# Optimization experiments

Hardware: AMD Instinct MI355X
Metric: run time of the kernel (lower is better)

## Reference

```python
import jax, jax.numpy as jnp
import numpy as np

B, T, D, H = 4, 2048, 1024, 16
HD = D // H

def setup_inputs() -> dict:
    key = jax.random.key(0)
    ks = jax.random.split(key, 5)
    s = 0.02
    return {
        "x": jax.random.normal(ks[0], (B, T, D), dtype=jnp.float32),
        "w_qkv": jax.random.normal(ks[1], (D, 3 * D), dtype=jnp.float32) * s,
        "b_qkv": jax.random.normal(ks[2], (3 * D,), dtype=jnp.float32) * s,
        "w_proj": jax.random.normal(ks[3], (D, D), dtype=jnp.float32) * s,
        "b_proj": jax.random.normal(ks[4], (D,), dtype=jnp.float32) * s,
    }

def reference(x, w_qkv, b_qkv, w_proj, b_proj):
    b, t, c = x.shape
    h, hd = H, HD
    scale = hd ** -0.5
    qkv = x @ w_qkv + b_qkv                       # [B,T,3D]
    qkv = qkv.reshape(b, t, 3, h, hd)
    q, k, v = qkv[:, :, 0], qkv[:, :, 1], qkv[:, :, 2]   # [B,T,H,HD]
    # scores [B,H,T,T]
    att = jnp.einsum('bqhd,bkhd->bhqk', q, k) * scale
    causal = jnp.tril(jnp.ones((t, t), dtype=bool))
    att = jnp.where(causal[None, None], att, -jnp.inf)
    w = jax.nn.softmax(att, axis=-1)
    out = jnp.einsum('bhqk,bkhd->bqhd', w, v).reshape(b, t, c)
    return out @ w_proj + b_proj
```

## Files before the change

### kernel.cpp

```cpp
#include <hip/hip_runtime.h>
#include <hip/hip_bf16.h>
#include <cstdint>

#define BB 4
#define TT 2048
#define DD 1024
#define HH 16
#define HD 64
#define MM (BB*TT)
#define NQKV (3*DD)
#define QSCALE 0.18033688f
#define NQT 16

typedef __bf16 bf16;
typedef __bf16 bf16x8 __attribute__((ext_vector_type(8)));
typedef float f32x4 __attribute__((ext_vector_type(4)));

#define AS1 __attribute__((address_space(1)))
#define AS3 __attribute__((address_space(3)))

__device__ __forceinline__ void gload_lds16(const void* g, void* l) {
  __builtin_amdgcn_global_load_lds((const AS1 uint32_t*)g, (AS3 uint32_t*)l, 16, 0, 0);
}

__global__ void k_prep(const float* __restrict__ x, bf16* __restrict__ xb,
                       const float* __restrict__ wqkv, bf16* __restrict__ wqkvT,
                       const float* __restrict__ wproj, bf16* __restrict__ wprojT) {
  __shared__ float tile[32][33];
  const int bid = blockIdx.x;
  if (bid < 8192) {
    const int i = bid * 256 + threadIdx.x;
    float4 v = ((const float4*)x)[i];
    ushort4 o;
    o.x = __builtin_bit_cast(unsigned short, (bf16)v.x);
    o.y = __builtin_bit_cast(unsigned short, (bf16)v.y);
    o.z = __builtin_bit_cast(unsigned short, (bf16)v.z);
    o.w = __builtin_bit_cast(unsigned short, (bf16)v.w);
    ((ushort4*)xb)[i] = o;
    return;
  }
  const float* in; bf16* out; int R, C, c0, r0;
  if (bid < 8192 + 3072) {
    const int id = bid - 8192;
    in = wqkv; out = wqkvT; R = DD; C = NQKV;
    c0 = (id % 96) * 32; r0 = (id / 96) * 32;
  } else {
    const int id = bid - 8192 - 3072;
    in = wproj; out = wprojT; R = DD; C = DD;
    c0 = (id % 32) * 32; r0 = (id / 32) * 32;
  }
  const int tx = threadIdx.x & 31, ty = threadIdx.x >> 5;
#pragma unroll
  for (int i = 0; i < 32; i += 8)
    tile[ty + i][tx] = in[(long)(r0 + ty + i) * C + c0 + tx];
  __syncthreads();
#pragma unroll
  for (int i = 0; i < 32; i += 8)
    out[(long)(c0 + ty + i) * R + r0 + tx] = (bf16)tile[tx][ty + i];
}

template <int EPI>
__global__ __launch_bounds__(256) void k_gemm(
    const bf16* __restrict__ A, const bf16* __restrict__ Bt,
    const float* __restrict__ bias, float* __restrict__ fout,
    bf16* __restrict__ q_out, bf16* __restrict__ k_out, bf16* __restrict__ v_out,
    int K) {
  __shared__ bf16 sm[2 * 128 * 64];
  bf16* const As = sm;
  bf16* const Bs = sm + 128 * 64;
  const int tid = threadIdx.x;
  const int m0 = blockIdx.x * 128;
  const int n0 = blockIdx.y * 128;
  const int wv = tid >> 6, lane = tid & 63;
  const int g = lane >> 4, lr = lane & 15;
  const int wm = (wv >> 1) * 64, wn = (wv & 1) * 64;
  const int sr = tid >> 3, sc = tid & 7;
  f32x4 acc[4][4] = {};

  for (int k0 = 0; k0 < K; k0 += 64) {
#pragma unroll
    for (int p = 0; p < 4; ++p) {
      const int row = p * 32 + sr;
      const int chunk = sc ^ (row & 7);
      gload_lds16(A + ((long)(m0 + row) * K + k0 + (chunk << 3)),
                  As + (row << 6) + (sc << 3));
      gload_lds16(Bt + ((long)(n0 + row) * K + k0 + (chunk << 3)),
                  Bs + (row << 6) + (sc << 3));
    }
    __syncthreads();
#pragma unroll
    for (int kf = 0; kf < 2; ++kf) {
      bf16x8 af[4], bfr[4];
#pragma unroll
      for (int mf = 0; mf < 4; ++mf) {
        const int row = wm + mf * 16 + lr;
        af[mf] = *(const bf16x8*)((const char*)As +
                 (((row << 7) + (kf << 6) + (g << 4)) ^ ((row & 7) << 4)));
      }
#pragma unroll
      for (int nf = 0; nf < 4; ++nf) {
        const int row = wn + nf * 16 + lr;
        bfr[nf] = *(const bf16x8*)((const char*)Bs +
                 (((row << 7) + (kf << 6) + (g << 4)) ^ ((row & 7) << 4)));
      }
#pragma unroll
      for (int mf = 0; mf < 4; ++mf)
#pragma unroll
        for (int nf = 0; nf < 4; ++nf)
          acc[mf][nf] = __builtin_amdgcn_mfma_f32_16x16x32_bf16(af[mf], bfr[nf],
                                                                acc[mf][nf], 0, 0, 0);
    }
    __syncthreads();
  }

  if (EPI == 0) {
    const int sel = n0 >> 10;
    const int d0 = n0 & 1023;
    const int b = m0 >> 11;
    const int t0 = m0 & 2047;
    const int h0 = d0 >> 6;
    if (sel < 2) {
      const float qs = (sel == 0) ? QSCALE : 1.0f;
      bf16* Cs = sm;
#pragma unroll
      for (int nf = 0; nf < 4; ++nf) {
        const int col = wn + nf * 16 + lr;
        const float bv = bias[n0 + col];
#pragma unroll
        for (int mf = 0; mf < 4; ++mf)
#pragma unroll
          for (int j = 0; j < 4; ++j) {
            const int row = wm + mf * 16 + g * 4 + j;
            const float v = (acc[mf][nf][j] + bv) * qs;
            const int cp = (col >> 3) ^ (((row >> 2) & 3) << 1);
            Cs[(row << 7) + (cp << 3) + (col & 7)] = (bf16)v;
          }
      }
      __syncthreads();
      bf16* dst = (sel == 0) ? q_out : k_out;
#pragma unroll
      for (int i = 0; i < 8; ++i) {
        const int cid = (i << 8) + tid;
        const int hh = cid >> 10;
        const int r  = (cid >> 3) & 127;
        const int ck = cid & 7;
        const int cp = ((hh << 3) + ck) ^ (((r >> 2) & 3) << 1);
        const bf16x8 vv = *(const bf16x8*)&Cs[(r << 7) + (cp << 3)];
        const long off = ((((long)b * HH + h0 + hh) * TT + t0 + r) << 6) + (ck << 3);
        *(bf16x8*)(dst + off) = vv;
      }
    } else {
      bf16* Cs = sm;
#pragma unroll
      for (int nf = 0; nf < 4; ++nf) {
        const int col = wn + nf * 16 + lr;
        const float bv = bias[n0 + col];
#pragma unroll
        for (int mf = 0; mf < 4; ++mf) {
          const int row0 = wm + mf * 16 + g * 4;
          ushort4 pk;
          pk.x = __builtin_bit_cast(unsigned short, (bf16)(acc[mf][nf][0] + bv));
          pk.y = __builtin_bit_cast(unsigned short, (bf16)(acc[mf][nf][1] + bv));
          pk.z = __builtin_bit_cast(unsigned short, (bf16)(acc[mf][nf][2] + bv));
          pk.w = __builtin_bit_cast(unsigned short, (bf16)(acc[mf][nf][3] + bv));
          *(ushort4*)((char*)Cs + ((col << 8) + ((row0 << 1) ^ ((col & 7) << 4)))) = pk;
        }
      }
      __syncthreads();
#pragma unroll
      for (int i = 0; i < 8; ++i) {
        const int cid = (i << 8) + tid;
        const int c  = cid >> 4;
        const int ck = cid & 15;
        const bf16x8 vv = *(const bf16x8*)((const char*)Cs +
                           ((c << 8) + ((ck << 4) ^ ((c & 7) << 4))));
        const int hh = c >> 6, hd = c & 63;
        const long off = (((long)b * HH + h0 + hh) * HD + hd) * TT + t0 + (ck << 3);
        *(bf16x8*)(v_out + off) = vv;
      }
    }
  } else {
    float* Cf = (float*)sm;
#pragma unroll
    for (int pass = 0; pass < 2; ++pass) {
      __syncthreads();
      if ((wm >> 6) == pass) {
#pragma unroll
        for (int nf = 0; nf < 4; ++nf) {
          const int col = wn + nf * 16 + lr;
          const float bv = bias[n0 + col];
#pragma unroll
          for (int mf = 0; mf < 4; ++mf)
#pragma unroll
            for (int j = 0; j < 4; ++j) {
              const int row = mf * 16 + g * 4 + j;
              const int cp = (col >> 2) ^ (((row >> 2) & 3) << 1);
              Cf[(row << 7) + (cp << 2) + (col & 3)] = acc[mf][nf][j] + bv;
            }
        }
      }
      __syncthreads();
#pragma unroll
      for (int i = 0; i < 8; ++i) {
        const int cid = (i << 8) + tid;
        const int r  = cid >> 5;
        const int ck = cid & 31;
        const int cp = ck ^ (((r >> 2) & 3) << 1);
        const float4 vv = *(const float4*)&Cf[(r << 7) + (cp << 2)];
        const long rowm = m0 + (pass << 6) + r;
        *(float4*)&fout[rowm * DD + n0 + (ck << 2)] = vv;
      }
    }
  }
}

template <bool MASKED>
__device__ __forceinline__ void attn_tile(
    const bf16* __restrict__ Kt, const bf16* __restrict__ Vt,
    bf16* __restrict__ Pw, const bf16x8 (&qf)[2][2],
    f32x4 (&acc)[2][4], f32x4 (&ls)[2],
    int rowbase, int kv0, int g, int lr, bf16x8 ones) {
  f32x4 s[2][4] = {};
#pragma unroll
  for (int kf = 0; kf < 2; ++kf) {
    bf16x8 bfr[4];
#pragma unroll
    for (int nf = 0; nf < 4; ++nf) {
      const int row = nf * 16 + lr;
      bfr[nf] = *(const bf16x8*)((const char*)Kt +
               (((row << 7) + (kf << 6) + (g << 4)) ^ ((row & 7) << 4)));
    }
#pragma unroll
    for (int mf = 0; mf < 2; ++mf)
#pragma unroll
      for (int nf = 0; nf < 4; ++nf)
        s[mf][nf] = __builtin_amdgcn_mfma_f32_16x16x32_bf16(qf[mf][kf], bfr[nf],
                                                            s[mf][nf], 0, 0, 0);
  }
#pragma unroll
  for (int mf = 0; mf < 2; ++mf) {
#pragma unroll
    for (int nf = 0; nf < 4; ++nf) {
      const int col = kv0 + nf * 16 + lr;
#pragma unroll
      for (int j = 0; j < 4; ++j) {
        float p;
        if (MASKED) {
          const int rowq = rowbase + mf * 16 + g * 4 + j;
          p = (col <= rowq) ? __builtin_amdgcn_exp2f(s[mf][nf][j]) : 0.f;
        } else {
          p = __builtin_amdgcn_exp2f(s[mf][nf][j]);
        }
        const int prow = mf * 16 + g * 4 + j;
        const int pcol = nf * 16 + lr;
        *(bf16*)((char*)Pw +
                 (((prow << 7) + (pcol << 1)) ^ ((prow & 7) << 4))) = (bf16)p;
      }
    }
  }
#pragma unroll
  for (int kf = 0; kf < 2; ++kf) {
    bf16x8 pa[2], vb[4];
#pragma unroll
    for (int mf = 0; mf < 2; ++mf) {
      const int row = mf * 16 + lr;
      pa[mf] = *(const bf16x8*)((const char*)Pw +
               (((row << 7) + (kf << 6) + (g << 4)) ^ ((row & 7) << 4)));
    }
#pragma unroll
    for (int nf = 0; nf < 4; ++nf) {
      const int row = nf * 16 + lr;
      vb[nf] = *(const bf16x8*)((const char*)Vt +
               (((row << 7) + (kf << 6) + (g << 4)) ^ ((row & 7) << 4)));
    }
#pragma unroll
    for (int mf = 0; mf < 2; ++mf)
      ls[mf] = __builtin_amdgcn_mfma_f32_16x16x32_bf16(pa[mf], ones, ls[mf], 0, 0, 0);
#pragma unroll
    for (int mf = 0; mf < 2; ++mf)
#pragma unroll
      for (int nf = 0; nf < 4; ++nf)
        acc[mf][nf] = __builtin_amdgcn_mfma_f32_16x16x32_bf16(pa[mf], vb[nf],
                                                              acc[mf][nf], 0, 0, 0);
  }
}

__global__ __launch_bounds__(256, 2) void k_attn(
    const bf16* __restrict__ Q, const bf16* __restrict__ K,
    const bf16* __restrict__ Vt, bf16* __restrict__ O) {
  __shared__ bf16 Ks[2][64 * 64];
  __shared__ bf16 Vs[2][64 * 64];
  __shared__ bf16 Ps[4][32 * 64];
  const int tid = threadIdx.x;
  const int d = blockIdx.y * gridDim.x + blockIdx.x;
  const int w = (d & 7) * 64 + (d >> 3);
  const int qa = w & 7, qb = NQT - 1 - qa;
  const int bh = w >> 3;
  const int b = bh >> 4, h = bh & 15;
  const int wv = tid >> 6, lane = tid & 63;
  const int g = lane >> 4, lr = lane & 15;
  const int ra = qa * 128 + wv * 32;
  const int rb = qb * 128 + wv * 32;
  const bf16* Qb = Q + (long)bh * TT * HD;
  const bf16* Kb = K + (long)bh * TT * HD;
  const bf16* Vb = Vt + (long)bh * HD * TT;
  bf16* Pw = &Ps[wv][0];

  bf16x8 ones;
#pragma unroll
  for (int i = 0; i < 8; ++i) ones[i] = (bf16)1.0f;

  bf16x8 qfa[2][2], qfb[2][2];
#pragma unroll
  for (int mf = 0; mf < 2; ++mf)
#pragma unroll
    for (int kf = 0; kf < 2; ++kf) {
      qfa[mf][kf] = *(const bf16x8*)(Qb + ((long)(ra + mf * 16 + lr) << 6) +
                                     kf * 32 + g * 8);
      qfb[mf][kf] = *(const bf16x8*)(Qb + ((long)(rb + mf * 16 + lr) << 6) +
                                     kf * 32 + g * 8);
    }

  f32x4 acca[2][4] = {}, accb[2][4] = {};
  f32x4 lsa[2] = {}, lsb[2] = {};

  const int sr = tid >> 3, sc = tid & 7;
  const int nkv = 2 * qb + 2;

  auto STAGE = [&](int buf, int kt) {
    const int kv0 = kt * 64;
#pragma unroll
    for (int p = 0; p < 2; ++p) {
      const int row = p * 32 + sr;
      const int chunk = sc ^ (row & 7);
      gload_lds16(Kb + ((long)(kv0 + row) << 6) + (chunk << 3),
                  &Ks[buf][(row << 6) + (sc << 3)]);
      gload_lds16(Vb + (long)row * TT + kv0 + (chunk << 3),
                  &Vs[buf][(row << 6) + (sc << 3)]);
    }
  };

  STAGE(0, 0);
  __syncthreads();

  int cur = 0;
  for (int kt = 0; kt < nkv; ++kt) {
    const int kv0 = kt * 64;
    if (kt + 1 < nkv) STAGE(cur ^ 1, kt + 1);

    const bf16* Kt  = &Ks[cur][0];
    const bf16* Vtl = &Vs[cur][0];
    if (kv0 + 63 <= ra)
      attn_tile<false>(Kt, Vtl, Pw, qfa, acca, lsa, ra, kv0, g, lr, ones);
    else if (kv0 <= ra + 31)
      attn_tile<true >(Kt, Vtl, Pw, qfa, acca, lsa, ra, kv0, g, lr, ones);
    if (kv0 + 63 <= rb)
      attn_tile<false>(Kt, Vtl, Pw, qfb, accb, lsb, rb, kv0, g, lr, ones);
    else if (kv0 <= rb + 31)
      attn_tile<true >(Kt, Vtl, Pw, qfb, accb, lsb, rb, kv0, g, lr, ones);

    __syncthreads();
    cur ^= 1;
  }

#pragma unroll
  for (int mf = 0; mf < 2; ++mf) {
    float inva[4], invb[4];
#pragma unroll
    for (int j = 0; j < 4; ++j) {
      inva[j] = 1.0f / lsa[mf][j];
      invb[j] = 1.0f / lsb[mf][j];
    }
#pragma unroll
    for (int nf = 0; nf < 4; ++nf) {
      const int col = h * 64 + nf * 16 + lr;
#pragma unroll
      for (int j = 0; j < 4; ++j) {
        const int ta = ra + mf * 16 + g * 4 + j;
        const int tb = rb + mf * 16 + g * 4 + j;
        O[(((long)b * TT + ta) << 10) + col] = (bf16)(acca[mf][nf][j] * inva[j]);
        O[(((long)b * TT + tb) << 10) + col] = (bf16)(accb[mf][nf][j] * invb[j]);
      }
    }
  }
}

extern "C" void kernel_launch(void* const* d_in, const int* in_sizes, int n_in,
                              void* d_out, int out_size, void* d_ws, size_t ws_size,
                              hipStream_t stream) {
  (void)in_sizes; (void)n_in; (void)out_size; (void)ws_size;
  const float* x      = (const float*)d_in[0];
  const float* w_qkv  = (const float*)d_in[1];
  const float* b_qkv  = (const float*)d_in[2];
  const float* w_proj = (const float*)d_in[3];
  const float* b_proj = (const float*)d_in[4];
  float* out = (float*)d_out;

  bf16* ws = (bf16*)d_ws;
  const long NX = (long)MM * DD;
  bf16* xb     = ws;
  bf16* wqkvT  = xb + NX;
  bf16* wprojT = wqkvT + (long)NQKV * DD;
  bf16* Qb     = wprojT + (long)DD * DD;
  bf16* Kb     = Qb + NX;
  bf16* Vtb    = Kb + NX;
  bf16* attout = xb;

  k_prep<<<8192 + 3072 + 1024, 256, 0, stream>>>(x, xb, w_qkv, wqkvT, w_proj, wprojT);
  k_gemm<0><<<dim3(MM / 128, NQKV / 128), 256, 0, stream>>>(
      xb, wqkvT, b_qkv, nullptr, Qb, Kb, Vtb, DD);
  k_attn<<<dim3(NQT / 2, BB * HH), 256, 0, stream>>>(Qb, Kb, Vtb, attout);
  k_gemm<1><<<dim3(MM / 128, DD / 128), 256, 0, stream>>>(
      attout, wprojT, b_proj, out, nullptr, nullptr, nullptr, DD);
}
```

Before: 165.6 us.

## Triple-buffer GEMM K-loop with async LDS loads and 256x128 tiles

Rewrites the bf16 GEMM used for the QKV and output projections. Tiles grow to 256x128 with 8 waves, and the K loop is triple-buffered: global-to-LDS loads for step k+2 are issued while step k computes, synchronised with explicit vmcnt waits and barriers. MFMA bursts run at raised priority. The goal is to hide global load latency and raise MFMA utilisation, in exchange for more LDS use (144KB per block), hardcoded K=1024, and epilogues rewritten for the larger tile.

```diff
diff --git a/kernel.cpp b/kernel.cpp
--- a/kernel.cpp
+++ b/kernel.cpp
@@ -11,6 +11,7 @@
 #define NQKV (3*DD)
 #define QSCALE 0.18033688f
 #define NQT 16
+#define NKT 16
 
 typedef __bf16 bf16;
 typedef __bf16 bf16x8 __attribute__((ext_vector_type(8)));
@@ -60,57 +61,105 @@
 }
 
 template <int EPI>
-__global__ __launch_bounds__(256) void k_gemm(
+__global__ __launch_bounds__(512, 2) void k_gemm(
     const bf16* __restrict__ A, const bf16* __restrict__ Bt,
     const float* __restrict__ bias, float* __restrict__ fout,
-    bf16* __restrict__ q_out, bf16* __restrict__ k_out, bf16* __restrict__ v_out,
-    int K) {
-  __shared__ bf16 sm[2 * 128 * 64];
-  bf16* const As = sm;
-  bf16* const Bs = sm + 128 * 64;
+    bf16* __restrict__ q_out, bf16* __restrict__ k_out, bf16* __restrict__ v_out) {
+  __shared__ bf16 sm[3 * 24576];
   const int tid = threadIdx.x;
-  const int m0 = blockIdx.x * 128;
+  const int m0 = blockIdx.x * 256;
   const int n0 = blockIdx.y * 128;
-  const int wv = tid >> 6, lane = tid & 63;
+  const int wid = tid >> 6, lane = tid & 63;
   const int g = lane >> 4, lr = lane & 15;
-  const int wm = (wv >> 1) * 64, wn = (wv & 1) * 64;
+  const int wr = wid >> 1, wc = wid & 1;
   const int sr = tid >> 3, sc = tid & 7;
+
+  auto STAGE = [&](int kt, int buf) {
+    bf16* As = sm + buf * 24576;
+    bf16* Bs = As + 16384;
+    const long k0 = (long)kt << 6;
+#pragma unroll
+    for (int p = 0; p < 4; ++p) {
+      const int row = p * 64 + sr;
+      const int chunk = sc ^ (row & 7);
+      gload_lds16(A + (((long)(m0 + row)) << 10) + k0 + (chunk << 3),
+                  As + (row << 6) + (sc << 3));
+    }
+#pragma unroll
+    for (int p = 0; p < 2; ++p) {
+      const int row = p * 64 + sr;
+      const int chunk = sc ^ (row & 7);
+      gload_lds16(Bt + (((long)(n0 + row)) << 10) + k0 + (chunk << 3),
+                  Bs + (row << 6) + (sc << 3));
+    }
+  };
+
   f32x4 acc[4][4] = {};
 
-  for (int k0 = 0; k0 < K; k0 += 64) {
-#pragma unroll
-    for (int p = 0; p < 4; ++p) {
-      const int row = p * 32 + sr;
-      const int chunk = sc ^ (row & 7);
-      gload_lds16(A + ((long)(m0 + row) * K + k0 + (chunk << 3)),
-                  As + (row << 6) + (sc << 3));
-      gload_lds16(Bt + ((long)(n0 + row) * K + k0 + (chunk << 3)),
-                  Bs + (row << 6) + (sc << 3));
-    }
-    __syncthreads();
-#pragma unroll
-    for (int kf = 0; kf < 2; ++kf) {
-      bf16x8 af[4], bfr[4];
-#pragma unroll
-      for (int mf = 0; mf < 4; ++mf) {
-        const int row = wm + mf * 16 + lr;
-        af[mf] = *(const bf16x8*)((const char*)As +
-                 (((row << 7) + (kf << 6) + (g << 4)) ^ ((row & 7) << 4)));
-      }
-#pragma unroll
-      for (int nf = 0; nf < 4; ++nf) {
-        const int row = wn + nf * 16 + lr;
-        bfr[nf] = *(const bf16x8*)((const char*)Bs +
-                 (((row << 7) + (kf << 6) + (g << 4)) ^ ((row & 7) << 4)));
-      }
-#pragma unroll
-      for (int mf = 0; mf < 4; ++mf)
-#pragma unroll
-        for (int nf = 0; nf < 4; ++nf)
-          acc[mf][nf] = __builtin_amdgcn_mfma_f32_16x16x32_bf16(af[mf], bfr[nf],
-                                                                acc[mf][nf], 0, 0, 0);
-    }
-    __syncthreads();
+  STAGE(0, 0);
+  STAGE(1, 1);
+  asm volatile("s_waitcnt vmcnt(6)" ::: "memory");
+  asm volatile("s_barrier" ::: "memory");
+
+  int b0 = 0, b1 = 1, b2 = 2;
+  for (int kt = 0; kt < NKT; ++kt) {
+    const bf16* As = sm + b0 * 24576;
+    const bf16* Bs = As + 16384;
+    if (kt + 2 < NKT) STAGE(kt + 2, b2);
+
+    bf16x8 af[4][2], bfr[2][2];
+#pragma unroll
+    for (int fm = 0; fm < 4; ++fm)
+#pragma unroll
+      for (int ks = 0; ks < 2; ++ks) {
+        const int row = wr * 64 + fm * 16 + lr;
+        af[fm][ks] = *(const bf16x8*)((const char*)As +
+                     (((row << 7) + (ks << 6) + (g << 4)) ^ ((row & 7) << 4)));
+      }
+#pragma unroll
+    for (int fn = 0; fn < 2; ++fn)
+#pragma unroll
+      for (int ks = 0; ks < 2; ++ks) {
+        const int row = wc * 64 + fn * 16 + lr;
+        bfr[fn][ks] = *(const bf16x8*)((const char*)Bs +
+                      (((row << 7) + (ks << 6) + (g << 4)) ^ ((row & 7) << 4)));
+      }
+    asm volatile("s_barrier" ::: "memory");
+    __builtin_amdgcn_s_setprio(1);
+#pragma unroll
+    for (int ks = 0; ks < 2; ++ks)
+#pragma unroll
+      for (int fm = 0; fm < 4; ++fm)
+#pragma unroll
+        for (int fn = 0; fn < 2; ++fn)
+          acc[fm][fn] = __builtin_amdgcn_mfma_f32_16x16x32_bf16(
+              af[fm][ks], bfr[fn][ks], acc[fm][fn], 0, 0, 0);
+    __builtin_amdgcn_s_setprio(0);
+    asm volatile("s_barrier" ::: "memory");
+
+#pragma unroll
+    for (int fn = 0; fn < 2; ++fn)
+#pragma unroll
+      for (int ks = 0; ks < 2; ++ks) {
+        const int row = wc * 64 + (fn + 2) * 16 + lr;
+        bfr[fn][ks] = *(const bf16x8*)((const char*)Bs +
+                      (((row << 7) + (ks << 6) + (g << 4)) ^ ((row & 7) << 4)));
+      }
+    asm volatile("s_barrier" ::: "memory");
+    __builtin_amdgcn_s_setprio(1);
+#pragma unroll
+    for (int ks = 0; ks < 2; ++ks)
+#pragma unroll
+      for (int fm = 0; fm < 4; ++fm)
+#pragma unroll
+        for (int fn = 0; fn < 2; ++fn)
+          acc[fm][fn + 2] = __builtin_amdgcn_mfma_f32_16x16x32_bf16(
+              af[fm][ks], bfr[fn][ks], acc[fm][fn + 2], 0, 0, 0);
+    __builtin_amdgcn_s_setprio(0);
+    if (kt + 2 < NKT) asm volatile("s_waitcnt vmcnt(6)" ::: "memory");
+    else              asm volatile("s_waitcnt vmcnt(0)" ::: "memory");
+    asm volatile("s_barrier" ::: "memory");
+    const int t = b0; b0 = b1; b1 = b2; b2 = t;
   }
 
   if (EPI == 0) {
@@ -123,15 +172,15 @@
       const float qs = (sel == 0) ? QSCALE : 1.0f;
       bf16* Cs = sm;
 #pragma unroll
-      for (int nf = 0; nf < 4; ++nf) {
-        const int col = wn + nf * 16 + lr;
+      for (int fn = 0; fn < 4; ++fn) {
+        const int col = wc * 64 + fn * 16 + lr;
         const float bv = bias[n0 + col];
 #pragma unroll
-        for (int mf = 0; mf < 4; ++mf)
+        for (int fm = 0; fm < 4; ++fm)
 #pragma unroll
           for (int j = 0; j < 4; ++j) {
-            const int row = wm + mf * 16 + g * 4 + j;
-            const float v = (acc[mf][nf][j] + bv) * qs;
+            const int row = wr * 64 + fm * 16 + g * 4 + j;
+            const float v = (acc[fm][fn][j] + bv) * qs;
             const int cp = (col >> 3) ^ (((row >> 2) & 3) << 1);
             Cs[(row << 7) + (cp << 3) + (col & 7)] = (bf16)v;
           }
@@ -140,11 +189,12 @@
       bf16* dst = (sel == 0) ? q_out : k_out;
 #pragma unroll
       for (int i = 0; i < 8; ++i) {
-        const int cid = (i << 8) + tid;
-        const int hh = cid >> 10;
-        const int r  = (cid >> 3) & 127;
-        const int ck = cid & 7;
-        const int cp = ((hh << 3) + ck) ^ (((r >> 2) & 3) << 1);
+        const int cid = (i << 9) + tid;
+        const int r   = cid >> 4;
+        const int ckf = cid & 15;
+        const int hh  = ckf >> 3;
+        const int ck  = ckf & 7;
+        const int cp  = ckf ^ (((r >> 2) & 3) << 1);
         const bf16x8 vv = *(const bf16x8*)&Cs[(r << 7) + (cp << 3)];
         const long off = ((((long)b * HH + h0 + hh) * TT + t0 + r) << 6) + (ck << 3);
         *(bf16x8*)(dst + off) = vv;
@@ -152,28 +202,28 @@
     } else {
       bf16* Cs = sm;
 #pragma unroll
-      for (int nf = 0; nf < 4; ++nf) {
-        const int col = wn + nf * 16 + lr;
+      for (int fn = 0; fn < 4; ++fn) {
+        const int col = wc * 64 + fn * 16 + lr;
         const float bv = bias[n0 + col];
 #pragma unroll
-        for (int mf = 0; mf < 4; ++mf) {
-          const int row0 = wm + mf * 16 + g * 4;
+        for (int fm = 0; fm < 4; ++fm) {
+          const int row0 = wr * 64 + fm * 16 + g * 4;
           ushort4 pk;
-          pk.x = __builtin_bit_cast(unsigned short, (bf16)(acc[mf][nf][0] + bv));
-          pk.y = __builtin_bit_cast(unsigned short, (bf16)(acc[mf][nf][1] + bv));
-          pk.z = __builtin_bit_cast(unsigned short, (bf16)(acc[mf][nf][2] + bv));
-          pk.w = __builtin_bit_cast(unsigned short, (bf16)(acc[mf][nf][3] + bv));
-          *(ushort4*)((char*)Cs + ((col << 8) + ((row0 << 1) ^ ((col & 7) << 4)))) = pk;
+          pk.x = __builtin_bit_cast(unsigned short, (bf16)(acc[fm][fn][0] + bv));
+          pk.y = __builtin_bit_cast(unsigned short, (bf16)(acc[fm][fn][1] + bv));
+          pk.z = __builtin_bit_cast(unsigned short, (bf16)(acc[fm][fn][2] + bv));
+          pk.w = __builtin_bit_cast(unsigned short, (bf16)(acc[fm][fn][3] + bv));
+          *(ushort4*)((char*)Cs + ((col << 9) + ((row0 << 1) ^ ((col & 7) << 4)))) = pk;
         }
       }
       __syncthreads();
 #pragma unroll
       for (int i = 0; i < 8; ++i) {
-        const int cid = (i << 8) + tid;
-        const int c  = cid >> 4;
-        const int ck = cid & 15;
+        const int cid = (i << 9) + tid;
+        const int c  = cid >> 5;
+        const int ck = cid & 31;
         const bf16x8 vv = *(const bf16x8*)((const char*)Cs +
-                           ((c << 8) + ((ck << 4) ^ ((c & 7) << 4))));
+                           ((c << 9) + ((ck << 4) ^ ((c & 7) << 4))));
         const int hh = c >> 6, hd = c & 63;
         const long off = (((long)b * HH + h0 + hh) * HD + hd) * TT + t0 + (ck << 3);
         *(bf16x8*)(v_out + off) = vv;
@@ -182,34 +232,27 @@
   } else {
     float* Cf = (float*)sm;
 #pragma unroll
-    for (int pass = 0; pass < 2; ++pass) {
-      __syncthreads();
-      if ((wm >> 6) == pass) {
-#pragma unroll
-        for (int nf = 0; nf < 4; ++nf) {
-          const int col = wn + nf * 16 + lr;
-          const float bv = bias[n0 + col];
-#pragma unroll
-          for (int mf = 0; mf < 4; ++mf)
-#pragma unroll
-            for (int j = 0; j < 4; ++j) {
-              const int row = mf * 16 + g * 4 + j;
-              const int cp = (col >> 2) ^ (((row >> 2) & 3) << 1);
-              Cf[(row << 7) + (cp << 2) + (col & 3)] = acc[mf][nf][j] + bv;
-            }
+    for (int fn = 0; fn < 4; ++fn) {
+      const int col = wc * 64 + fn * 16 + lr;
+      const float bv = bias[n0 + col];
+#pragma unroll
+      for (int fm = 0; fm < 4; ++fm)
+#pragma unroll
+        for (int j = 0; j < 4; ++j) {
+          const int row = wr * 64 + fm * 16 + g * 4 + j;
+          const int cp = (col >> 2) ^ (((row >> 2) & 3) << 1);
+          Cf[(row << 7) + (cp << 2) + (col & 3)] = acc[fm][fn][j] + bv;
         }
-      }
-      __syncthreads();
-#pragma unroll
-      for (int i = 0; i < 8; ++i) {
-        const int cid = (i << 8) + tid;
-        const int r  = cid >> 5;
-        const int ck = cid & 31;
-        const int cp = ck ^ (((r >> 2) & 3) << 1);
-        const float4 vv = *(const float4*)&Cf[(r << 7) + (cp << 2)];
-        const long rowm = m0 + (pass << 6) + r;
-        *(float4*)&fout[rowm * DD + n0 + (ck << 2)] = vv;
-      }
+    }
+    __syncthreads();
+#pragma unroll
+    for (int i = 0; i < 16; ++i) {
+      const int cid = (i << 9) + tid;
+      const int r   = cid >> 5;
+      const int ckf = cid & 31;
+      const int cp  = ckf ^ (((r >> 2) & 3) << 1);
+      const float4 vv = *(const float4*)&Cf[(r << 7) + (cp << 2)];
+      *(float4*)&fout[(long)(m0 + r) * DD + n0 + (ckf << 2)] = vv;
     }
   }
 }
@@ -407,9 +450,9 @@
   bf16* attout = xb;
 
   k_prep<<<8192 + 3072 + 1024, 256, 0, stream>>>(x, xb, w_qkv, wqkvT, w_proj, wprojT);
-  k_gemm<0><<<dim3(MM / 128, NQKV / 128), 256, 0, stream>>>(
-      xb, wqkvT, b_qkv, nullptr, Qb, Kb, Vtb, DD);
+  k_gemm<0><<<dim3(MM / 256, NQKV / 128), 512, 0, stream>>>(
+      xb, wqkvT, b_qkv, nullptr, Qb, Kb, Vtb);
   k_attn<<<dim3(NQT / 2, BB * HH), 256, 0, stream>>>(Qb, Kb, Vtb, attout);
-  k_gemm<1><<<dim3(MM / 128, DD / 128), 256, 0, stream>>>(
-      attout, wprojT, b_proj, out, nullptr, nullptr, nullptr, DD);
-}
+  k_gemm<1><<<dim3(MM / 256, DD / 128), 512, 0, stream>>>(
+      attout, wprojT, b_proj, out, nullptr, nullptr, nullptr);
+}
```

Result: no change. 162.5 us, median of 2 (-1.8%).
